# Optimization experiments

Hardware: AMD Instinct MI355X
Metric: run time of the kernel (lower is better)

## Reference

```python
import jax, jax.numpy as jnp
from jax import lax
import numpy as np

PAD_IDX = 0
NEG = -1e30  # mask value for max-pool over invalid positions


def setup_inputs() -> dict:
    key = jax.random.key(0)
    ks = jax.random.split(key, 12)
    B, S, D, F = 1024, 128, 768, 4
    x = jax.random.randint(ks[0], (B, S), 0, 32000)
    hidden = jax.random.normal(ks[1], (B, S, D), dtype=jnp.float32)
    sc = 0.02
    w2 = jax.random.normal(ks[2], (F, D, 2), dtype=jnp.float32) * sc
    b2 = jax.random.normal(ks[3], (F,), dtype=jnp.float32) * sc
    w3 = jax.random.normal(ks[4], (F, D, 3), dtype=jnp.float32) * sc
    b3 = jax.random.normal(ks[5], (F,), dtype=jnp.float32) * sc
    w4 = jax.random.normal(ks[6], (F, D, 4), dtype=jnp.float32) * sc
    b4 = jax.random.normal(ks[7], (F,), dtype=jnp.float32) * sc
    w5 = jax.random.normal(ks[8], (F, D, 5), dtype=jnp.float32) * sc
    b5 = jax.random.normal(ks[9], (F,), dtype=jnp.float32) * sc
    fc_w = jax.random.normal(ks[10], (1, 4 * F), dtype=jnp.float32) * sc
    fc_b = jax.random.normal(ks[11], (1,), dtype=jnp.float32) * sc
    return {"x": x, "hidden": hidden, "w2": w2, "b2": b2, "w3": w3, "b3": b3,
            "w4": w4, "b4": b4, "w5": w5, "b5": b5, "fc_w": fc_w, "fc_b": fc_b}


def _ragged_conv_maxpool(hT, lengths, w, b, k, S):
    # hT: [B, D, S] compacted (non-pad tokens first); conv = torch Conv1d semantics
    conv = lax.conv_general_dilated(hT, w, (1,), 'VALID',
                                    dimension_numbers=('NCW', 'OIW', 'NCW'))
    conv = conv + b[None, :, None]          # [B, F, S-k+1]
    t = jnp.arange(S - k + 1)
    valid = t[None, :] < (lengths - k + 1)[:, None]  # [B, S-k+1]
    return jnp.max(jnp.where(valid[:, None, :], conv, NEG), axis=-1)  # [B, F]


def reference(x, hidden, w2, b2, w3, b3, w4, b4, w5, b5, fc_w, fc_b):
    B, S, D = hidden.shape
    is_pad = (x == PAD_IDX)
    # stable argsort compacts non-pad positions to the front, preserving order
    order = jnp.argsort(is_pad, axis=1, stable=True)           # [B, S]
    lengths = jnp.sum(~is_pad, axis=1)                          # [B]
    hc = jnp.take_along_axis(hidden, order[:, :, None], axis=1)  # [B, S, D]
    hT = hc.transpose(0, 2, 1)                                  # [B, D, S]
    pooled = [
        _ragged_conv_maxpool(hT, lengths, w2, b2, 2, S),
        _ragged_conv_maxpool(hT, lengths, w3, b3, 3, S),
        _ragged_conv_maxpool(hT, lengths, w4, b4, 4, S),
        _ragged_conv_maxpool(hT, lengths, w5, b5, 5, S),
    ]
    feats = jnp.concatenate(pooled, axis=-1)                    # [B, 4F]
    logits = feats @ fc_w.T + fc_b                              # [B, 1]
    return jax.nn.sigmoid(logits).squeeze(-1)                   # [B]
```

## Files before the change

### kernel.cpp

```cpp
#include <hip/hip_runtime.h>
#include <hip/hip_bf16.h>
#include <cstdint>

typedef __attribute__((ext_vector_type(8))) short bf16x8;
typedef __attribute__((ext_vector_type(4))) float f32x4;

#define NEGV -1e30f

__device__ __forceinline__ unsigned short f2bf(float f) {
    unsigned u = __builtin_bit_cast(unsigned, f);
    u += 0x7fffu + ((u >> 16) & 1u);
    return (unsigned short)(u >> 16);
}

__global__ void prep_w_kernel(const float* __restrict__ w2, const float* __restrict__ w3,
                              const float* __restrict__ w4, const float* __restrict__ w5,
                              unsigned short* __restrict__ Wb) {
    int id = blockIdx.x * blockDim.x + threadIdx.x;
    if (id >= 24 * 4 * 64 * 8) return;
    int j     = id & 7;
    int lane  = (id >> 3) & 63;
    int nt    = (id >> 9) & 3;
    int kstep = id >> 11;
    int kglob = kstep * 32 + ((lane >> 4) & 3) * 8 + j;
    int c     = nt * 16 + (lane & 15);
    float v = 0.f;
    if (c < 56) {
        int k, off; const float* w;
        if (c < 8)       { k = 2; off = 0;  w = w2; }
        else if (c < 20) { k = 3; off = 8;  w = w3; }
        else if (c < 36) { k = 4; off = 20; w = w4; }
        else             { k = 5; off = 36; w = w5; }
        int jj = (c - off) >> 2;
        int f  = (c - off) & 3;
        v = w[f * 768 * k + kglob * k + jj];
    }
    Wb[id] = f2bf(v);
}

__global__ void __launch_bounds__(256)
cnn_main_kernel(const int* __restrict__ x, const float* __restrict__ hidden,
                const unsigned short* __restrict__ Wb,
                const float* __restrict__ b2, const float* __restrict__ b3,
                const float* __restrict__ b4, const float* __restrict__ b5,
                const float* __restrict__ fc_w, const float* __restrict__ fc_b,
                float* __restrict__ out) {
    __shared__ int   order_s[128];
    __shared__ int   cnt_w[2];
    __shared__ int   len_s;
    __shared__ float P[128][65];
    __shared__ float redbuf[16][17];
    __shared__ float feats[16];

    const int b   = blockIdx.x;
    const int tid = threadIdx.x;

    int nonpad = 0, pre = 0;
    if (tid < 128) {
        order_s[tid] = 127;
        nonpad = (x[b * 128 + tid] != 0) ? 1 : 0;
        unsigned long long mask = __ballot(nonpad);
        int lane = tid & 63;
        pre = __popcll(mask & ((1ull << lane) - 1ull));
        if (lane == 0) cnt_w[tid >> 6] = (int)__popcll(mask);
    }
    __syncthreads();
    if (tid < 128) {
        if (nonpad) {
            int base = (tid >= 64) ? cnt_w[0] : 0;
            order_s[base + pre] = tid;
        }
        if (tid == 0) len_s = cnt_w[0] + cnt_w[1];
    }
    __syncthreads();

    const int w    = tid >> 6;
    const int lane = tid & 63;
    const int lrow = lane & 15;
    const int quad = lane >> 4;

    const int t0 = w * 32 + lrow;
    const int t1 = t0 + 16;
    const int s0 = order_s[t0];
    const int s1 = order_s[t1];
    const float* pa0 = hidden + (size_t)(b * 128 + s0) * 768 + quad * 8;
    const float* pa1 = hidden + (size_t)(b * 128 + s1) * 768 + quad * 8;
    const bf16x8* bp = (const bf16x8*)(Wb + lane * 8);

    f32x4 acc[2][4];
#pragma unroll
    for (int mt = 0; mt < 2; ++mt)
#pragma unroll
        for (int nt = 0; nt < 4; ++nt) acc[mt][nt] = (f32x4){0.f, 0.f, 0.f, 0.f};

#pragma unroll 2
    for (int ks = 0; ks < 24; ++ks) {
        f32x4 a0lo = *(const f32x4*)(pa0 + ks * 32);
        f32x4 a0hi = *(const f32x4*)(pa0 + ks * 32 + 4);
        f32x4 a1lo = *(const f32x4*)(pa1 + ks * 32);
        f32x4 a1hi = *(const f32x4*)(pa1 + ks * 32 + 4);
        bf16x8 af0, af1;
#pragma unroll
        for (int j = 0; j < 4; ++j) {
            af0[j]     = (short)f2bf(a0lo[j]);
            af0[j + 4] = (short)f2bf(a0hi[j]);
            af1[j]     = (short)f2bf(a1lo[j]);
            af1[j + 4] = (short)f2bf(a1hi[j]);
        }
        bf16x8 bf[4];
#pragma unroll
        for (int nt = 0; nt < 4; ++nt) bf[nt] = bp[ks * 256 + nt * 64];
#pragma unroll
        for (int nt = 0; nt < 4; ++nt) {
            acc[0][nt] = __builtin_amdgcn_mfma_f32_16x16x32_bf16(af0, bf[nt], acc[0][nt], 0, 0, 0);
            acc[1][nt] = __builtin_amdgcn_mfma_f32_16x16x32_bf16(af1, bf[nt], acc[1][nt], 0, 0, 0);
        }
    }

#pragma unroll
    for (int mt = 0; mt < 2; ++mt)
#pragma unroll
        for (int nt = 0; nt < 4; ++nt)
#pragma unroll
            for (int r = 0; r < 4; ++r) {
                int t = w * 32 + mt * 16 + quad * 4 + r;
                int c = nt * 16 + lrow;
                P[t][c] = acc[mt][nt][r];
            }
    __syncthreads();

    {
        const int p   = tid >> 4;
        const int l16 = tid & 15;
        const int kg  = p >> 2;
        const int kk  = 2 + kg;
        const int off = (kg == 0) ? 0 : (kg == 1) ? 8 : (kg == 2) ? 20 : 36;
        const int f   = p & 3;
        const int len = len_s;
        float lm = NEGV;
        for (int t = l16; t <= len - kk; t += 16) {
            float v = 0.f;
#pragma unroll 5
            for (int j = 0; j < kk; ++j) v += P[t + j][off + j * 4 + f];
            lm = fmaxf(lm, v);
        }
        redbuf[p][l16] = lm;
    }
    __syncthreads();
    if (tid < 16) {
        float m = redbuf[tid][0];
#pragma unroll
        for (int i = 1; i < 16; ++i) m = fmaxf(m, redbuf[tid][i]);
        const float* bk = (tid < 4) ? b2 : (tid < 8) ? b3 : (tid < 12) ? b4 : b5;
        feats[tid] = m + bk[tid & 3];
    }
    __syncthreads();
    if (tid == 0) {
        float logit = fc_b[0];
#pragma unroll
        for (int i = 0; i < 16; ++i) logit += feats[i] * fc_w[i];
        out[b] = 1.f / (1.f + expf(-logit));
    }
}

extern "C" void kernel_launch(void* const* d_in, const int* in_sizes, int n_in,
                              void* d_out, int out_size, void* d_ws, size_t ws_size,
                              hipStream_t stream) {
    const int*   x      = (const int*)d_in[0];
    const float* hidden = (const float*)d_in[1];
    const float* w2     = (const float*)d_in[2];
    const float* b2     = (const float*)d_in[3];
    const float* w3     = (const float*)d_in[4];
    const float* b3     = (const float*)d_in[5];
    const float* w4     = (const float*)d_in[6];
    const float* b4     = (const float*)d_in[7];
    const float* w5     = (const float*)d_in[8];
    const float* b5     = (const float*)d_in[9];
    const float* fc_w   = (const float*)d_in[10];
    const float* fc_b   = (const float*)d_in[11];
    float* out = (float*)d_out;

    unsigned short* Wb = (unsigned short*)d_ws;

    prep_w_kernel<<<(24 * 4 * 64 * 8 + 255) / 256, 256, 0, stream>>>(w2, w3, w4, w5, Wb);
    cnn_main_kernel<<<1024, 256, 0, stream>>>(x, hidden, Wb, b2, b3, b4, b5, fc_w, fc_b, out);
}
```

Measured before the change: 551.2 us.

## Use 1024-thread blocks with one M-tile and two N-tiles per wave

Raises the block size from 256 to 1024 threads so that 16 waves split the per-batch GEMM. Each wave handles one 16-row token tile and two of the four 16-column filter tiles, instead of two row tiles and all four column tiles. The pooling stage now gives one wave per (kernel size, filter) pair and reduces with wave shuffles instead of a shared-memory reduction buffer. The aim is more memory-level parallelism per CU to hide the latency of the bandwidth-bound hidden-state loads. The cost is that each A row is loaded and converted twice, by two waves, and the launch bound asks for 8 waves per SIMD, which limits registers.

```diff
diff --git a/kernel.cpp b/kernel.cpp
--- a/kernel.cpp
+++ b/kernel.cpp
@@ -38,7 +38,7 @@
     Wb[id] = f2bf(v);
 }
 
-__global__ void __launch_bounds__(256)
+__global__ void __launch_bounds__(1024, 8)
 cnn_main_kernel(const int* __restrict__ x, const float* __restrict__ hidden,
                 const unsigned short* __restrict__ Wb,
                 const float* __restrict__ b2, const float* __restrict__ b3,
@@ -49,7 +49,6 @@
     __shared__ int   cnt_w[2];
     __shared__ int   len_s;
     __shared__ float P[128][65];
-    __shared__ float redbuf[16][17];
     __shared__ float feats[16];
 
     const int b   = blockIdx.x;
@@ -78,81 +77,60 @@
     const int lane = tid & 63;
     const int lrow = lane & 15;
     const int quad = lane >> 4;
+    const int mt   = w & 7;
+    const int nh   = w >> 3;
 
-    const int t0 = w * 32 + lrow;
-    const int t1 = t0 + 16;
-    const int s0 = order_s[t0];
-    const int s1 = order_s[t1];
-    const float* pa0 = hidden + (size_t)(b * 128 + s0) * 768 + quad * 8;
-    const float* pa1 = hidden + (size_t)(b * 128 + s1) * 768 + quad * 8;
-    const bf16x8* bp = (const bf16x8*)(Wb + lane * 8);
+    const int trow = mt * 16 + lrow;
+    const int s    = order_s[trow];
+    const float* pa = hidden + (size_t)(b * 128 + s) * 768 + quad * 8;
+    const bf16x8* bp = (const bf16x8*)Wb + (nh * 2) * 64 + lane;
 
-    f32x4 acc[2][4];
-#pragma unroll
-    for (int mt = 0; mt < 2; ++mt)
-#pragma unroll
-        for (int nt = 0; nt < 4; ++nt) acc[mt][nt] = (f32x4){0.f, 0.f, 0.f, 0.f};
+    f32x4 acc0 = (f32x4){0.f, 0.f, 0.f, 0.f};
+    f32x4 acc1 = (f32x4){0.f, 0.f, 0.f, 0.f};
 
-#pragma unroll 2
+#pragma unroll 3
     for (int ks = 0; ks < 24; ++ks) {
-        f32x4 a0lo = *(const f32x4*)(pa0 + ks * 32);
-        f32x4 a0hi = *(const f32x4*)(pa0 + ks * 32 + 4);
-        f32x4 a1lo = *(const f32x4*)(pa1 + ks * 32);
-        f32x4 a1hi = *(const f32x4*)(pa1 + ks * 32 + 4);
-        bf16x8 af0, af1;
+        f32x4 alo = *(const f32x4*)(pa + ks * 32);
+        f32x4 ahi = *(const f32x4*)(pa + ks * 32 + 4);
+        bf16x8 bf0 = bp[ks * 256];
+        bf16x8 bf1 = bp[ks * 256 + 64];
+        bf16x8 af;
 #pragma unroll
         for (int j = 0; j < 4; ++j) {
-            af0[j]     = (short)f2bf(a0lo[j]);
-            af0[j + 4] = (short)f2bf(a0hi[j]);
-            af1[j]     = (short)f2bf(a1lo[j]);
-            af1[j + 4] = (short)f2bf(a1hi[j]);
+            af[j]     = (short)f2bf(alo[j]);
+            af[j + 4] = (short)f2bf(ahi[j]);
         }
-        bf16x8 bf[4];
-#pragma unroll
-        for (int nt = 0; nt < 4; ++nt) bf[nt] = bp[ks * 256 + nt * 64];
-#pragma unroll
-        for (int nt = 0; nt < 4; ++nt) {
-            acc[0][nt] = __builtin_amdgcn_mfma_f32_16x16x32_bf16(af0, bf[nt], acc[0][nt], 0, 0, 0);
-            acc[1][nt] = __builtin_amdgcn_mfma_f32_16x16x32_bf16(af1, bf[nt], acc[1][nt], 0, 0, 0);
-        }
+        acc0 = __builtin_amdgcn_mfma_f32_16x16x32_bf16(af, bf0, acc0, 0, 0, 0);
+        acc1 = __builtin_amdgcn_mfma_f32_16x16x32_bf16(af, bf1, acc1, 0, 0, 0);
     }
 
 #pragma unroll
-    for (int mt = 0; mt < 2; ++mt)
-#pragma unroll
-        for (int nt = 0; nt < 4; ++nt)
-#pragma unroll
-            for (int r = 0; r < 4; ++r) {
-                int t = w * 32 + mt * 16 + quad * 4 + r;
-                int c = nt * 16 + lrow;
-                P[t][c] = acc[mt][nt][r];
-            }
+    for (int r = 0; r < 4; ++r) {
+        int t = mt * 16 + quad * 4 + r;
+        P[t][(nh * 2) * 16 + lrow]     = acc0[r];
+        P[t][(nh * 2 + 1) * 16 + lrow] = acc1[r];
+    }
     __syncthreads();
 
     {
-        const int p   = tid >> 4;
-        const int l16 = tid & 15;
-        const int kg  = p >> 2;
+        const int kg  = w >> 2;
         const int kk  = 2 + kg;
         const int off = (kg == 0) ? 0 : (kg == 1) ? 8 : (kg == 2) ? 20 : 36;
-        const int f   = p & 3;
+        const int f   = w & 3;
         const int len = len_s;
         float lm = NEGV;
-        for (int t = l16; t <= len - kk; t += 16) {
+        for (int t = lane; t <= len - kk; t += 64) {
             float v = 0.f;
 #pragma unroll 5
             for (int j = 0; j < kk; ++j) v += P[t + j][off + j * 4 + f];
             lm = fmaxf(lm, v);
         }
-        redbuf[p][l16] = lm;
-    }
-    __syncthreads();
-    if (tid < 16) {
-        float m = redbuf[tid][0];
 #pragma unroll
-        for (int i = 1; i < 16; ++i) m = fmaxf(m, redbuf[tid][i]);
-        const float* bk = (tid < 4) ? b2 : (tid < 8) ? b3 : (tid < 12) ? b4 : b5;
-        feats[tid] = m + bk[tid & 3];
+        for (int o = 32; o > 0; o >>= 1) lm = fmaxf(lm, __shfl_down(lm, o));
+        if (lane == 0) {
+            const float* bk = (kg == 0) ? b2 : (kg == 1) ? b3 : (kg == 2) ? b4 : b5;
+            feats[w] = lm + bk[f];
+        }
     }
     __syncthreads();
     if (tid == 0) {
@@ -183,5 +161,5 @@
     unsigned short* Wb = (unsigned short*)d_ws;
 
     prep_w_kernel<<<(24 * 4 * 64 * 8 + 255) / 256, 256, 0, stream>>>(w2, w3, w4, w5, Wb);
-    cnn_main_kernel<<<1024, 256, 0, stream>>>(x, hidden, Wb, b2, b3, b4, b5, fc_w, fc_b, out);
+    cnn_main_kernel<<<1024, 1024, 0, stream>>>(x, hidden, Wb, b2, b3, b4, b5, fc_w, fc_b, out);
 }
```

Measured after the change: 576.2 us. +4.5%, slower.
